# Performance work log

Measured on AMD Instinct MI355X. Metric: run time of the kernel, lower is better.

The kernel has to match this reference:

```python
import jax, jax.numpy as jnp
import numpy as np

OUT_IMG = 256
OUT_MSK = 64


def _src_coords(n_out, size):
    # F.interpolate bilinear align_corners=False source coordinates, clamped to edge
    sizef = size.astype(jnp.float32)
    t = (jnp.arange(n_out, dtype=jnp.float32) + 0.5) * (sizef / n_out) - 0.5
    t = jnp.clip(t, 0.0, sizef - 1.0)
    t0 = jnp.floor(t).astype(jnp.int32)
    t1 = jnp.minimum(t0 + 1, size - 1)
    return t0, t1, t - t0.astype(jnp.float32)


def _per_sample(x_img, x_msk, x_bg, pad, sel, color):
    # x_img [3,H,W] float, x_msk [H,W] bool, x_bg [3,Hb,Wb], pad [4] int (l,r,t,b)
    H, W = x_msk.shape
    ys = jnp.any(x_msk, axis=1)
    xs = jnp.any(x_msk, axis=0)
    iy = jnp.arange(H)
    ix = jnp.arange(W)
    miny = jnp.min(jnp.where(ys, iy, H))
    maxy = jnp.max(jnp.where(ys, iy, -1))
    minx = jnp.min(jnp.where(xs, ix, W))
    maxx = jnp.max(jnp.where(xs, ix, -1))
    h = maxy - miny + 1
    w = maxx - minx + 1
    left, right, top, bot = pad[0], pad[1], pad[2], pad[3]
    Hp = h + top + bot   # padded crop height
    Wp = w + left + right  # padded crop width
    # background: real bg image or solid random color (c[ii][-1] > 2 branch)
    bg_sel = jnp.where(sel > 2, x_bg, jnp.broadcast_to(color[:, None, None], x_bg.shape))

    def mask_at(P, Q):
        # value of the padded-cropped mask at integer padded coords (P, Q)
        in_crop = (P >= top) & (P < top + h) & (Q >= left) & (Q < left + w)
        r = jnp.clip(miny + P - top, 0, H - 1)
        c = jnp.clip(minx + Q - left, 0, W - 1)
        return in_crop & x_msk[r, c], r, c

    def sample_img(py, px):
        # composited padded image at integer coords (py x px grid) -> [3,Ho,Wo]
        P = py[:, None]
        Q = px[None, :]
        m, r, c = mask_at(P, Q)
        iv = x_img[:, r, c]
        bv = bg_sel[:, P, Q]
        return jnp.where(m[None], iv, bv)

    def sample_msk(py, px):
        m, _, _ = mask_at(py[:, None], px[None, :])
        return m.astype(jnp.float32)

    def bilinear(sample_fn, n_out, ch_leading):
        y0, y1, wy = _src_coords(n_out, Hp)
        x0, x1, wx = _src_coords(n_out, Wp)
        s00 = sample_fn(y0, x0)
        s01 = sample_fn(y0, x1)
        s10 = sample_fn(y1, x0)
        s11 = sample_fn(y1, x1)
        wy_ = wy[:, None]
        wx_ = wx[None, :]
        if ch_leading:
            wy_ = wy_[None]
            wx_ = wx_[None]
        top_row = s00 * (1.0 - wx_) + s01 * wx_
        bot_row = s10 * (1.0 - wx_) + s11 * wx_
        return top_row * (1.0 - wy_) + bot_row * wy_

    img_out = bilinear(sample_img, OUT_IMG, True)        # [3,256,256]
    msk_out = bilinear(sample_msk, OUT_MSK, False)[None]  # [1,64,64]
    return img_out, msk_out


def _rgb_to_hsv(x):
    r, g, b = x[:, 0], x[:, 1], x[:, 2]
    mx = jnp.max(x, axis=1)
    mn = jnp.min(x, axis=1)
    d = mx - mn
    ds = jnp.where(d > 0, d, 1.0)
    hr = ((g - b) / ds) % 6.0
    hg = (b - r) / ds + 2.0
    hb = (r - g) / ds + 4.0
    hch = jnp.where(mx == r, hr, jnp.where(mx == g, hg, hb)) / 6.0
    hch = jnp.where(d > 0, hch, 0.0)
    s = jnp.where(mx > 0, d / jnp.where(mx > 0, mx, 1.0), 0.0)
    return hch, s, mx


def _hsv_to_rgb(hch, s, v):
    h6 = hch * 6.0
    i = jnp.floor(h6)
    f = h6 - i
    p = v * (1.0 - s)
    q = v * (1.0 - f * s)
    t = v * (1.0 - (1.0 - f) * s)
    im = i.astype(jnp.int32) % 6
    conds = [im == 0, im == 1, im == 2, im == 3, im == 4, im == 5]
    r = jnp.select(conds, [v, q, p, p, t, v])
    g = jnp.select(conds, [t, v, v, q, p, p])
    b = jnp.select(conds, [p, p, t, v, v, q])
    return jnp.stack([r, g, b], axis=1)


def _color_jitter(img, jit):
    # ColorJitter(0.1, 0.1, 0.1, 0.1) with explicit per-sample factors
    b = (0.9 + 0.2 * jit[:, 0])[:, None, None, None]
    c = (0.9 + 0.2 * jit[:, 1])[:, None, None, None]
    s = (0.9 + 0.2 * jit[:, 2])[:, None, None, None]
    hd = (-0.1 + 0.2 * jit[:, 3])[:, None, None]
    img = jnp.clip(img * b, 0.0, 1.0)
    gray = (0.299 * img[:, 0] + 0.587 * img[:, 1] + 0.114 * img[:, 2])[:, None]
    mean = jnp.mean(gray, axis=(2, 3), keepdims=True)
    img = jnp.clip(c * img + (1.0 - c) * mean, 0.0, 1.0)
    gray = (0.299 * img[:, 0] + 0.587 * img[:, 1] + 0.114 * img[:, 2])[:, None]
    img = jnp.clip(s * img + (1.0 - s) * gray, 0.0, 1.0)
    hch, sa, v = _rgb_to_hsv(img)
    hch = (hch + hd) % 1.0
    return jnp.clip(_hsv_to_rgb(hch, sa, v), 0.0, 1.0)


def setup_inputs() -> dict:
    key = jax.random.key(0)
    ks = jax.random.split(key, 7)
    B, H, W = 64, 448, 448
    return {
        "img": jax.random.uniform(ks[0], (B, 3, H, W), jnp.float32),
        "ms": jax.random.uniform(ks[1], (B, 1, H, W), jnp.float32),
        "bg": jax.random.uniform(ks[2], (B, 3, H + 40, W + 40), jnp.float32),
        "pads": jax.random.randint(ks[3], (B, 4), 0, 20, jnp.int32),
        "csel": jax.random.randint(ks[4], (B,), 0, 20, jnp.int32),
        "rand_color": jax.random.uniform(ks[5], (B, 3), jnp.float32),
        "jitter": jax.random.uniform(ks[6], (B, 4), jnp.float32),
    }


def reference(img, ms, bg, pads, csel, rand_color, jitter):
    mask = ms[:, 0] > 0.5
    img_out, msk_out = jax.vmap(_per_sample)(img, mask, bg, pads, csel, rand_color)
    img_out = _color_jitter(img_out, jitter)
    return img_out, msk_out
```

## Files before the change

### kernel.cpp

```cpp
#include <hip/hip_runtime.h>

#define H_IN 448
#define W_IN 448
#define HW_IN (H_IN * W_IN)
#define BGW 488
#define BGHW (BGW * BGW)
#define OUTI 256
#define OUTI_PIX (OUTI * OUTI)
#define OUTM 64
#define B_SAMPLES 64
#define BBOX_CHUNKS 16
#define BBOX_ROWS (H_IN / BBOX_CHUNKS)

__device__ __forceinline__ float clamp01(float x) { return fminf(fmaxf(x, 0.f), 1.f); }
__device__ __forceinline__ int clampi(int x, int lo, int hi) { return min(max(x, lo), hi); }

__global__ void k_bbox(const float* __restrict__ ms, int* __restrict__ bbox) {
    int b = blockIdx.y;
    int chunk = blockIdx.x;
    const float4* m4 = (const float4*)(ms + (size_t)b * HW_IN + (size_t)chunk * BBOX_ROWS * W_IN);
    int miny = H_IN, maxy = -1, minx = W_IN, maxx = -1;
    const int N4 = BBOX_ROWS * (W_IN / 4);
    for (int i = threadIdx.x; i < N4; i += blockDim.x) {
        float4 v = m4[i];
        bool a0 = v.x > 0.5f, a1 = v.y > 0.5f, a2 = v.z > 0.5f, a3 = v.w > 0.5f;
        if (a0 | a1 | a2 | a3) {
            int y = chunk * BBOX_ROWS + i / (W_IN / 4);
            int xb = (i % (W_IN / 4)) * 4;
            miny = min(miny, y); maxy = max(maxy, y);
            if (a0) { minx = min(minx, xb);     maxx = max(maxx, xb); }
            if (a1) { minx = min(minx, xb + 1); maxx = max(maxx, xb + 1); }
            if (a2) { minx = min(minx, xb + 2); maxx = max(maxx, xb + 2); }
            if (a3) { minx = min(minx, xb + 3); maxx = max(maxx, xb + 3); }
        }
    }
    __shared__ int s[4];
    if (threadIdx.x == 0) { s[0] = H_IN; s[1] = -1; s[2] = W_IN; s[3] = -1; }
    __syncthreads();
    atomicMin(&s[0], miny); atomicMax(&s[1], maxy);
    atomicMin(&s[2], minx); atomicMax(&s[3], maxx);
    __syncthreads();
    if (threadIdx.x == 0) {
        atomicMin(&bbox[b * 4 + 0], s[0]);
        atomicMin(&bbox[b * 4 + 1], -s[1]);
        atomicMin(&bbox[b * 4 + 2], s[2]);
        atomicMin(&bbox[b * 4 + 3], -s[3]);
    }
}

struct Geo {
    int miny, minx, h, w, top, left, Hp, Wp;
};
__device__ __forceinline__ Geo load_geo(const int* __restrict__ bbox,
                                        const int* __restrict__ pads, int b) {
    Geo g;
    g.miny = bbox[b * 4 + 0];
    int maxy = -bbox[b * 4 + 1];
    g.minx = bbox[b * 4 + 2];
    int maxx = -bbox[b * 4 + 3];
    int left = pads[b * 4 + 0], right = pads[b * 4 + 1];
    int top = pads[b * 4 + 2], bot = pads[b * 4 + 3];
    g.h = maxy - g.miny + 1;
    g.w = maxx - g.minx + 1;
    g.top = top; g.left = left;
    g.Hp = g.h + top + bot;
    g.Wp = g.w + left + right;
    return g;
}

__device__ __forceinline__ void src_coord(int i, int n_out, int size,
                                          int& t0, int& t1, float& frac) {
    float sizef = (float)size;
    float t = (i + 0.5f) * (sizef / (float)n_out) - 0.5f;
    t = fminf(fmaxf(t, 0.f), sizef - 1.f);
    t0 = (int)floorf(t);
    t1 = min(t0 + 1, size - 1);
    frac = t - (float)t0;
}

__global__ void k_resize_img(const float* __restrict__ img, const float* __restrict__ ms,
                             const float* __restrict__ bg, const int* __restrict__ pads,
                             const int* __restrict__ csel, const float* __restrict__ rcol,
                             const float* __restrict__ jit, const int* __restrict__ bbox,
                             float* __restrict__ out, float* __restrict__ partials) {
    int b = blockIdx.y;
    int pix = blockIdx.x * blockDim.x + threadIdx.x;
    int oy = pix >> 8, ox = pix & 255;

    Geo g = load_geo(bbox, pads, b);
    bool useBg = csel[b] > 2;
    float c0 = rcol[b * 3 + 0], c1 = rcol[b * 3 + 1], c2 = rcol[b * 3 + 2];
    float bfac = 0.9f + 0.2f * jit[b * 4 + 0];

    int y0, y1, x0, x1; float wy, wx;
    src_coord(oy, OUTI, g.Hp, y0, y1, wy);
    src_coord(ox, OUTI, g.Wp, x0, x1, wx);

    const float* imB = img + (size_t)b * 3 * HW_IN;
    const float* msB = ms + (size_t)b * HW_IN;
    const float* bgB = bg + (size_t)b * 3 * BGHW;

    float acc0 = 0.f, acc1 = 0.f, acc2 = 0.f;
#pragma unroll
    for (int tap = 0; tap < 4; ++tap) {
        int P = (tap & 2) ? y1 : y0;
        int Q = (tap & 1) ? x1 : x0;
        float wgt = ((tap & 2) ? wy : 1.f - wy) * ((tap & 1) ? wx : 1.f - wx);
        bool in_crop = (P >= g.top) && (P < g.top + g.h) && (Q >= g.left) && (Q < g.left + g.w);
        int r = clampi(g.miny + P - g.top, 0, H_IN - 1);
        int c = clampi(g.minx + Q - g.left, 0, W_IN - 1);
        bool mm = in_crop && (msB[r * W_IN + c] > 0.5f);
        float v0, v1, v2;
        if (mm) {
            int o = r * W_IN + c;
            v0 = imB[o]; v1 = imB[HW_IN + o]; v2 = imB[2 * HW_IN + o];
        } else if (useBg) {
            int Pc = clampi(P, 0, BGW - 1), Qc = clampi(Q, 0, BGW - 1);
            int o = Pc * BGW + Qc;
            v0 = bgB[o]; v1 = bgB[BGHW + o]; v2 = bgB[2 * BGHW + o];
        } else {
            v0 = c0; v1 = c1; v2 = c2;
        }
        acc0 += wgt * v0; acc1 += wgt * v1; acc2 += wgt * v2;
    }
    float o0 = clamp01(acc0 * bfac);
    float o1 = clamp01(acc1 * bfac);
    float o2 = clamp01(acc2 * bfac);
    size_t o = (size_t)b * 3 * OUTI_PIX + pix;
    out[o] = o0;
    out[o + OUTI_PIX] = o1;
    out[o + 2 * OUTI_PIX] = o2;

    float gsum = 0.299f * o0 + 0.587f * o1 + 0.114f * o2;
#pragma unroll
    for (int off = 32; off > 0; off >>= 1) gsum += __shfl_down(gsum, off, 64);
    __shared__ float ls[4];
    int wid = threadIdx.x >> 6, lane = threadIdx.x & 63;
    if (lane == 0) ls[wid] = gsum;
    __syncthreads();
    if (threadIdx.x == 0)
        partials[b * 256 + blockIdx.x] = ls[0] + ls[1] + ls[2] + ls[3];
}

__global__ void k_resize_msk(const float* __restrict__ ms, const int* __restrict__ pads,
                             const int* __restrict__ bbox, float* __restrict__ outm) {
    int b = blockIdx.y;
    int pix = blockIdx.x * blockDim.x + threadIdx.x;
    int oy = pix >> 6, ox = pix & 63;

    Geo g = load_geo(bbox, pads, b);
    int y0, y1, x0, x1; float wy, wx;
    src_coord(oy, OUTM, g.Hp, y0, y1, wy);
    src_coord(ox, OUTM, g.Wp, x0, x1, wx);

    const float* msB = ms + (size_t)b * HW_IN;
    float acc = 0.f;
#pragma unroll
    for (int tap = 0; tap < 4; ++tap) {
        int P = (tap & 2) ? y1 : y0;
        int Q = (tap & 1) ? x1 : x0;
        float wgt = ((tap & 2) ? wy : 1.f - wy) * ((tap & 1) ? wx : 1.f - wx);
        bool in_crop = (P >= g.top) && (P < g.top + g.h) && (Q >= g.left) && (Q < g.left + g.w);
        int r = clampi(g.miny + P - g.top, 0, H_IN - 1);
        int c = clampi(g.minx + Q - g.left, 0, W_IN - 1);
        bool mm = in_crop && (msB[r * W_IN + c] > 0.5f);
        acc += wgt * (mm ? 1.f : 0.f);
    }
    outm[(size_t)b * (OUTM * OUTM) + pix] = acc;
}

__device__ __forceinline__ void jitter_px(float& r, float& g, float& bl,
                                          float cc, float ssf, float hd, float mean) {
    r = clamp01(cc * r + (1.f - cc) * mean);
    g = clamp01(cc * g + (1.f - cc) * mean);
    bl = clamp01(cc * bl + (1.f - cc) * mean);
    float gray = 0.299f * r + 0.587f * g + 0.114f * bl;
    r = clamp01(ssf * r + (1.f - ssf) * gray);
    g = clamp01(ssf * g + (1.f - ssf) * gray);
    bl = clamp01(ssf * bl + (1.f - ssf) * gray);
    float mx = fmaxf(r, fmaxf(g, bl));
    float mn = fminf(r, fminf(g, bl));
    float d = mx - mn;
    float dsv = (d > 0.f) ? d : 1.f;
    float hch;
    if (mx == r) {
        float t = (g - bl) / dsv;
        t = fmodf(t, 6.f);
        if (t < 0.f) t += 6.f;
        hch = t;
    } else if (mx == g) {
        hch = (bl - r) / dsv + 2.f;
    } else {
        hch = (r - g) / dsv + 4.f;
    }
    hch = (d > 0.f) ? hch * (1.f / 6.f) : 0.f;
    float sat = (mx > 0.f) ? d / mx : 0.f;
    float v = mx;
    float hh = hch + hd;
    hh -= floorf(hh);
    float h6 = hh * 6.f;
    float fi = floorf(h6);
    float f = h6 - fi;
    float pp = v * (1.f - sat);
    float q = v * (1.f - f * sat);
    float t = v * (1.f - (1.f - f) * sat);
    int im = ((int)fi) % 6;
    float ro, go, bo;
    switch (im) {
        case 0: ro = v;  go = t;  bo = pp; break;
        case 1: ro = q;  go = v;  bo = pp; break;
        case 2: ro = pp; go = v;  bo = t;  break;
        case 3: ro = pp; go = q;  bo = v;  break;
        case 4: ro = t;  go = pp; bo = v;  break;
        default: ro = v; go = pp; bo = q;  break;
    }
    r = clamp01(ro); g = clamp01(go); bl = clamp01(bo);
}

__global__ void k_jitter(float* __restrict__ io, const float* __restrict__ jit,
                         const float* __restrict__ partials) {
    int b = blockIdx.y;
    int tid = threadIdx.x;

    float pv = partials[b * 256 + tid];
#pragma unroll
    for (int off = 32; off > 0; off >>= 1) pv += __shfl_down(pv, off, 64);
    __shared__ float ls[4];
    int wid = tid >> 6, lane = tid & 63;
    if (lane == 0) ls[wid] = pv;
    __syncthreads();
    float mean = (ls[0] + ls[1] + ls[2] + ls[3]) * (1.f / (float)OUTI_PIX);

    float cc = 0.9f + 0.2f * jit[b * 4 + 1];
    float ssf = 0.9f + 0.2f * jit[b * 4 + 2];
    float hd = -0.1f + 0.2f * jit[b * 4 + 3];

    int idx4 = blockIdx.x * blockDim.x + tid;
    float4* pr = (float4*)(io + (size_t)b * 3 * OUTI_PIX) + idx4;
    float4* pg = pr + OUTI_PIX / 4;
    float4* pb = pr + 2 * (OUTI_PIX / 4);
    float4 r = *pr, g = *pg, bl = *pb;

    jitter_px(r.x, g.x, bl.x, cc, ssf, hd, mean);
    jitter_px(r.y, g.y, bl.y, cc, ssf, hd, mean);
    jitter_px(r.z, g.z, bl.z, cc, ssf, hd, mean);
    jitter_px(r.w, g.w, bl.w, cc, ssf, hd, mean);

    *pr = r; *pg = g; *pb = bl;
}

extern "C" void kernel_launch(void* const* d_in, const int* in_sizes, int n_in,
                              void* d_out, int out_size, void* d_ws, size_t ws_size,
                              hipStream_t stream) {
    const float* img = (const float*)d_in[0];
    const float* ms = (const float*)d_in[1];
    const float* bg = (const float*)d_in[2];
    const int* pads = (const int*)d_in[3];
    const int* csel = (const int*)d_in[4];
    const float* rcol = (const float*)d_in[5];
    const float* jit = (const float*)d_in[6];
    float* out = (float*)d_out;

    int* bbox = (int*)d_ws;
    float* partials = (float*)((char*)d_ws + B_SAMPLES * 4 * sizeof(int));
    float* outm = out + (size_t)B_SAMPLES * 3 * OUTI_PIX;

    hipMemsetAsync(bbox, 0x7F, B_SAMPLES * 4 * sizeof(int), stream);

    k_bbox<<<dim3(BBOX_CHUNKS, B_SAMPLES), 256, 0, stream>>>(ms, bbox);
    k_resize_img<<<dim3(OUTI_PIX / 256, B_SAMPLES), 256, 0, stream>>>(
        img, ms, bg, pads, csel, rcol, jit, bbox, out, partials);
    k_resize_msk<<<dim3((OUTM * OUTM) / 256, B_SAMPLES), 256, 0, stream>>>(ms, pads, bbox, outm);
    k_jitter<<<dim3(OUTI_PIX / 4 / 256, B_SAMPLES), 256, 0, stream>>>(out, jit, partials);
}
```

Before: 140.5 us.

## Stage two source rows per output row in LDS for image resize

Each block of the image resize kernel now handles one output row. It first loads the two source rows of mask, image (three channels) and, when used, background into shared memory with float4 loads. The bilinear taps then read from LDS instead of scattered global gathers, which cuts redundant global traffic and uncoalesced accesses. In exchange it copies full 448/488-wide rows even when the crop is narrow, adds about 20KB of LDS per block that may limit occupancy, and adds a barrier before compute.

```diff
diff --git a/kernel.cpp b/kernel.cpp
--- a/kernel.cpp
+++ b/kernel.cpp
@@ -78,46 +78,84 @@
     frac = t - (float)t0;
 }
 
-__global__ void k_resize_img(const float* __restrict__ img, const float* __restrict__ ms,
-                             const float* __restrict__ bg, const int* __restrict__ pads,
-                             const int* __restrict__ csel, const float* __restrict__ rcol,
-                             const float* __restrict__ jit, const int* __restrict__ bbox,
-                             float* __restrict__ out, float* __restrict__ partials) {
+__global__ void __launch_bounds__(256) k_resize_img(
+        const float* __restrict__ img, const float* __restrict__ ms,
+        const float* __restrict__ bg, const int* __restrict__ pads,
+        const int* __restrict__ csel, const float* __restrict__ rcol,
+        const float* __restrict__ jit, const int* __restrict__ bbox,
+        float* __restrict__ out, float* __restrict__ partials) {
     int b = blockIdx.y;
-    int pix = blockIdx.x * blockDim.x + threadIdx.x;
-    int oy = pix >> 8, ox = pix & 255;
+    int oy = blockIdx.x;
+    int tid = threadIdx.x;
 
     Geo g = load_geo(bbox, pads, b);
     bool useBg = csel[b] > 2;
     float c0 = rcol[b * 3 + 0], c1 = rcol[b * 3 + 1], c2 = rcol[b * 3 + 2];
     float bfac = 0.9f + 0.2f * jit[b * 4 + 0];
 
-    int y0, y1, x0, x1; float wy, wx;
+    int y0, y1; float wy;
     src_coord(oy, OUTI, g.Hp, y0, y1, wy);
-    src_coord(ox, OUTI, g.Wp, x0, x1, wx);
-
+    int r0 = clampi(g.miny + y0 - g.top, 0, H_IN - 1);
+    int r1 = clampi(g.miny + y1 - g.top, 0, H_IN - 1);
+    int P0 = clampi(y0, 0, BGW - 1);
+    int P1 = clampi(y1, 0, BGW - 1);
+    bool incy0 = (y0 >= g.top) && (y0 < g.top + g.h);
+    bool incy1 = (y1 >= g.top) && (y1 < g.top + g.h);
+
+    __shared__ float s_ms[2][W_IN];
+    __shared__ float s_im[2][3][W_IN];
+    __shared__ float s_bg[2][3][BGW];
+
+    const float* msB = ms + (size_t)b * HW_IN;
     const float* imB = img + (size_t)b * 3 * HW_IN;
-    const float* msB = ms + (size_t)b * HW_IN;
     const float* bgB = bg + (size_t)b * 3 * BGHW;
+
+    for (int item = tid; item < 8 * (W_IN / 4); item += 256) {
+        int plane = item / (W_IN / 4);
+        int idx = item - plane * (W_IN / 4);
+        const float* sp;
+        float* dp;
+        if (plane < 2) {
+            sp = msB + (size_t)(plane ? r1 : r0) * W_IN;
+            dp = s_ms[plane];
+        } else {
+            int q = plane - 2;
+            int ky = q / 3, ch = q - 3 * ky;
+            sp = imB + (size_t)ch * HW_IN + (size_t)(ky ? r1 : r0) * W_IN;
+            dp = &s_im[ky][ch][0];
+        }
+        ((float4*)dp)[idx] = ((const float4*)sp)[idx];
+    }
+    if (useBg) {
+        for (int item = tid; item < 6 * (BGW / 4); item += 256) {
+            int plane = item / (BGW / 4);
+            int idx = item - plane * (BGW / 4);
+            int ky = plane / 3, ch = plane - 3 * ky;
+            const float* sp = bgB + (size_t)ch * BGHW + (size_t)(ky ? P1 : P0) * BGW;
+            ((float4*)(&s_bg[ky][ch][0]))[idx] = ((const float4*)sp)[idx];
+        }
+    }
+    __syncthreads();
+
+    int x0, x1; float wx;
+    src_coord(tid, OUTI, g.Wp, x0, x1, wx);
 
     float acc0 = 0.f, acc1 = 0.f, acc2 = 0.f;
 #pragma unroll
     for (int tap = 0; tap < 4; ++tap) {
-        int P = (tap & 2) ? y1 : y0;
+        int ky = tap >> 1;
         int Q = (tap & 1) ? x1 : x0;
-        float wgt = ((tap & 2) ? wy : 1.f - wy) * ((tap & 1) ? wx : 1.f - wx);
-        bool in_crop = (P >= g.top) && (P < g.top + g.h) && (Q >= g.left) && (Q < g.left + g.w);
-        int r = clampi(g.miny + P - g.top, 0, H_IN - 1);
+        float wgt = (ky ? wy : 1.f - wy) * ((tap & 1) ? wx : 1.f - wx);
+        bool incy = ky ? incy1 : incy0;
+        bool in_crop = incy && (Q >= g.left) && (Q < g.left + g.w);
         int c = clampi(g.minx + Q - g.left, 0, W_IN - 1);
-        bool mm = in_crop && (msB[r * W_IN + c] > 0.5f);
+        bool mm = in_crop && (s_ms[ky][c] > 0.5f);
         float v0, v1, v2;
         if (mm) {
-            int o = r * W_IN + c;
-            v0 = imB[o]; v1 = imB[HW_IN + o]; v2 = imB[2 * HW_IN + o];
+            v0 = s_im[ky][0][c]; v1 = s_im[ky][1][c]; v2 = s_im[ky][2][c];
         } else if (useBg) {
-            int Pc = clampi(P, 0, BGW - 1), Qc = clampi(Q, 0, BGW - 1);
-            int o = Pc * BGW + Qc;
-            v0 = bgB[o]; v1 = bgB[BGHW + o]; v2 = bgB[2 * BGHW + o];
+            int Qc = clampi(Q, 0, BGW - 1);
+            v0 = s_bg[ky][0][Qc]; v1 = s_bg[ky][1][Qc]; v2 = s_bg[ky][2][Qc];
         } else {
             v0 = c0; v1 = c1; v2 = c2;
         }
@@ -126,7 +164,7 @@
     float o0 = clamp01(acc0 * bfac);
     float o1 = clamp01(acc1 * bfac);
     float o2 = clamp01(acc2 * bfac);
-    size_t o = (size_t)b * 3 * OUTI_PIX + pix;
+    size_t o = (size_t)b * 3 * OUTI_PIX + (size_t)oy * OUTI + tid;
     out[o] = o0;
     out[o + OUTI_PIX] = o1;
     out[o + 2 * OUTI_PIX] = o2;
@@ -135,11 +173,11 @@
 #pragma unroll
     for (int off = 32; off > 0; off >>= 1) gsum += __shfl_down(gsum, off, 64);
     __shared__ float ls[4];
-    int wid = threadIdx.x >> 6, lane = threadIdx.x & 63;
+    int wid = tid >> 6, lane = tid & 63;
     if (lane == 0) ls[wid] = gsum;
     __syncthreads();
-    if (threadIdx.x == 0)
-        partials[b * 256 + blockIdx.x] = ls[0] + ls[1] + ls[2] + ls[3];
+    if (tid == 0)
+        partials[b * 256 + oy] = ls[0] + ls[1] + ls[2] + ls[3];
 }
 
 __global__ void k_resize_msk(const float* __restrict__ ms, const int* __restrict__ pads,
@@ -268,7 +306,7 @@
     hipMemsetAsync(bbox, 0x7F, B_SAMPLES * 4 * sizeof(int), stream);
 
     k_bbox<<<dim3(BBOX_CHUNKS, B_SAMPLES), 256, 0, stream>>>(ms, bbox);
-    k_resize_img<<<dim3(OUTI_PIX / 256, B_SAMPLES), 256, 0, stream>>>(
+    k_resize_img<<<dim3(OUTI, B_SAMPLES), 256, 0, stream>>>(
         img, ms, bg, pads, csel, rcol, jit, bbox, out, partials);
     k_resize_msk<<<dim3((OUTM * OUTM) / 256, B_SAMPLES), 256, 0, stream>>>(ms, pads, bbox, outm);
     k_jitter<<<dim3(OUTI_PIX / 4 / 256, B_SAMPLES), 256, 0, stream>>>(out, jit, partials);
```

Result: faster. 134.6 us (-4.2%).
